# Kernel tuning notes

Hardware: AMD Instinct MI355X
Metric: run time of the kernel (lower is better)

## Reference

```python
import jax, jax.numpy as jnp
import numpy as np

B, T = 4, 2048
IN_H, OUT_H = 4096, 4096   # in_hidden_size = output features, out_hidden_size = input features (torch F.linear quirk)
RANK = 1024


def setup_inputs() -> dict:
    key = jax.random.key(0)
    kx, ku, ks, kv, kb = jax.random.split(key, 5)
    x = jax.random.normal(kx, (B, T, OUT_H), dtype=jnp.float32)
    U = jax.random.normal(ku, (IN_H, RANK), dtype=jnp.float32) * 0.02
    S = jax.random.uniform(ks, (RANK,), dtype=jnp.float32)
    V = jax.random.normal(kv, (OUT_H, RANK), dtype=jnp.float32) * 0.02
    bias = jax.random.normal(kb, (IN_H,), dtype=jnp.float32) * 0.01
    return {"x": x, "U": U, "S": S, "V": V, "bias": bias}


def reference(x, U, S, V, bias):
    # Faithful to torch: M = U @ diag(S) @ V.T  (shape [in_hidden, out_hidden]);
    # F.linear(x, M, bias) = x @ M.T + bias, so x:[...,out_hidden] -> out:[...,in_hidden]
    M = (U * S) @ V.T                     # [IN_H, OUT_H]; (U*S) == U @ diag(S)
    return jnp.einsum('bto,io->bti', x, M) + bias
```

## Files before the change

kernel.cpp:

```cpp
#include <hip/hip_runtime.h>
#include <stdint.h>

typedef __attribute__((ext_vector_type(4))) float  floatx4;
typedef __attribute__((ext_vector_type(8))) short  short8;
typedef __attribute__((ext_vector_type(8))) __bf16 bf16x8;

__device__ __forceinline__ unsigned short f2bf(float f) {
  unsigned int u = __builtin_bit_cast(unsigned int, f);
  u += 0x7fffu + ((u >> 16) & 1u);
  return (unsigned short)(u >> 16);
}

__global__ __launch_bounds__(256) void cast_x_kernel(const float* __restrict__ X,
                                                     unsigned short* __restrict__ Xb) {
  size_t i = ((size_t)blockIdx.x * 256 + threadIdx.x) * 8;
  const floatx4* p = (const floatx4*)(X + i);
  floatx4 a = p[0], b = p[1];
  union { unsigned short us[8]; short8 v; } o;
  o.us[0] = f2bf(a[0]); o.us[1] = f2bf(a[1]); o.us[2] = f2bf(a[2]); o.us[3] = f2bf(a[3]);
  o.us[4] = f2bf(b[0]); o.us[5] = f2bf(b[1]); o.us[6] = f2bf(b[2]); o.us[7] = f2bf(b[3]);
  *(short8*)(Xb + i) = o.v;
}

__global__ __launch_bounds__(256) void transpose_v_kernel(const float* __restrict__ V,
                                                          unsigned short* __restrict__ Vt,
                                                          int rows, int cols) {
  __shared__ float tile[32][33];
  int bx = blockIdx.x * 32;
  int by = blockIdx.y * 32;
  int tx = threadIdx.x & 31;
  int ty = threadIdx.x >> 5;
  for (int i = ty; i < 32; i += 8)
    tile[i][tx] = V[(size_t)(by + i) * cols + bx + tx];
  __syncthreads();
  for (int i = ty; i < 32; i += 8)
    Vt[(size_t)(bx + i) * rows + by + tx] = f2bf(tile[tx][i]);
}

__global__ __launch_bounds__(256) void prep_u_kernel(const float* __restrict__ U,
                                                     const float* __restrict__ S,
                                                     unsigned short* __restrict__ Ub,
                                                     unsigned int rankMask) {
  size_t i = ((size_t)blockIdx.x * 256 + threadIdx.x) * 4;
  floatx4 u = *(const floatx4*)(U + i);
  floatx4 s = *(const floatx4*)(S + (i & (size_t)rankMask));
  union { unsigned short us[4]; unsigned long long v; } o;
  o.us[0] = f2bf(u[0] * s[0]); o.us[1] = f2bf(u[1] * s[1]);
  o.us[2] = f2bf(u[2] * s[2]); o.us[3] = f2bf(u[3] * s[3]);
  *(unsigned long long*)(Ub + i) = o.v;
}

template <bool STORE_BF16>
__global__ __launch_bounds__(256, 2)
void gemm_bt_kernel(const unsigned short* __restrict__ A,
                    const unsigned short* __restrict__ Bt,
                    void* __restrict__ Cv,
                    const float* __restrict__ bias,
                    int M, int N, int K) {
  __shared__ unsigned short sA[128 * 32];
  __shared__ unsigned short sB[128 * 32];

  const int tid  = threadIdx.x;
  const int lane = tid & 63;
  const int wave = tid >> 6;
  const int wm = (wave >> 1) * 64;
  const int wn = (wave & 1) * 64;
  const int row0 = blockIdx.y * 128;
  const int col0 = blockIdx.x * 128;

  floatx4 acc[4][4];
  for (int i = 0; i < 4; ++i)
    for (int j = 0; j < 4; ++j)
      acc[i][j] = (floatx4){0.f, 0.f, 0.f, 0.f};

  const unsigned short* Ablk = A + (size_t)row0 * K;
  const unsigned short* Bblk = Bt + (size_t)col0 * K;

  const int r0 = tid >> 2,         c0 = (tid & 3) * 8;
  const int r1 = (256 + tid) >> 2, c1 = (tid & 3) * 8;
  const int base0 = (wave * 64) * 8;
  const int base1 = (256 + wave * 64) * 8;

  const int mrow = lane & 15;
  const int quad = lane >> 4;

  typedef const __attribute__((address_space(1))) void* gptr_t;
  typedef __attribute__((address_space(3))) void*       lptr_t;

  for (int k0 = 0; k0 < K; k0 += 32) {
    __builtin_amdgcn_global_load_lds((gptr_t)(Ablk + (size_t)r0 * K + k0 + c0),
                                     (lptr_t)(sA + base0), 16, 0, 0);
    __builtin_amdgcn_global_load_lds((gptr_t)(Ablk + (size_t)r1 * K + k0 + c1),
                                     (lptr_t)(sA + base1), 16, 0, 0);
    __builtin_amdgcn_global_load_lds((gptr_t)(Bblk + (size_t)r0 * K + k0 + c0),
                                     (lptr_t)(sB + base0), 16, 0, 0);
    __builtin_amdgcn_global_load_lds((gptr_t)(Bblk + (size_t)r1 * K + k0 + c1),
                                     (lptr_t)(sB + base1), 16, 0, 0);
    __syncthreads();

    bf16x8 af[4], bfr[4];
#pragma unroll
    for (int mi = 0; mi < 4; ++mi)
      af[mi] = __builtin_bit_cast(bf16x8,
                *(const short8*)(sA + (wm + mi * 16 + mrow) * 32 + quad * 8));
#pragma unroll
    for (int ni = 0; ni < 4; ++ni)
      bfr[ni] = __builtin_bit_cast(bf16x8,
                *(const short8*)(sB + (wn + ni * 16 + mrow) * 32 + quad * 8));
#pragma unroll
    for (int mi = 0; mi < 4; ++mi)
#pragma unroll
      for (int ni = 0; ni < 4; ++ni)
        acc[mi][ni] = __builtin_amdgcn_mfma_f32_16x16x32_bf16(af[mi], bfr[ni],
                                                              acc[mi][ni], 0, 0, 0);
    __syncthreads();
  }

  const int orow = row0 + wm + quad * 4;
  const int ocol = col0 + wn + mrow;
  if (STORE_BF16) {
    unsigned short* C = (unsigned short*)Cv;
#pragma unroll
    for (int mi = 0; mi < 4; ++mi)
#pragma unroll
      for (int r = 0; r < 4; ++r) {
        size_t rowoff = (size_t)(orow + mi * 16 + r) * N;
#pragma unroll
        for (int ni = 0; ni < 4; ++ni)
          C[rowoff + ocol + ni * 16] = f2bf(acc[mi][ni][r]);
      }
  } else {
    float* C = (float*)Cv;
    float bv[4];
#pragma unroll
    for (int ni = 0; ni < 4; ++ni) bv[ni] = bias[ocol + ni * 16];
#pragma unroll
    for (int mi = 0; mi < 4; ++mi)
#pragma unroll
      for (int r = 0; r < 4; ++r) {
        size_t rowoff = (size_t)(orow + mi * 16 + r) * N;
#pragma unroll
        for (int ni = 0; ni < 4; ++ni)
          C[rowoff + ocol + ni * 16] = acc[mi][ni][r] + bv[ni];
      }
  }
}

extern "C" void kernel_launch(void* const* d_in, const int* in_sizes, int n_in,
                              void* d_out, int out_size, void* d_ws, size_t ws_size,
                              hipStream_t stream) {
  const float* x    = (const float*)d_in[0];
  const float* U    = (const float*)d_in[1];
  const float* S    = (const float*)d_in[2];
  const float* V    = (const float*)d_in[3];
  const float* bias = (const float*)d_in[4];

  const int RANK = in_sizes[2];
  const int INH  = in_sizes[4];
  const int OUTH = in_sizes[3] / RANK;
  const int M    = in_sizes[0] / OUTH;

  unsigned short* Xb = (unsigned short*)d_ws;
  unsigned short* Vt = Xb + (size_t)M * OUTH;
  unsigned short* Ub = Vt + (size_t)RANK * OUTH;
  unsigned short* Yb = Ub + (size_t)INH * RANK;

  cast_x_kernel<<<(int)(((size_t)M * OUTH) / 2048), 256, 0, stream>>>(x, Xb);
  transpose_v_kernel<<<dim3(RANK / 32, OUTH / 32), 256, 0, stream>>>(V, Vt, OUTH, RANK);
  prep_u_kernel<<<(int)(((size_t)INH * RANK) / 1024), 256, 0, stream>>>(U, S, Ub,
                                                                        (unsigned)(RANK - 1));
  gemm_bt_kernel<true><<<dim3(RANK / 128, M / 128), 256, 0, stream>>>(
      Xb, Vt, (void*)Yb, nullptr, M, RANK, OUTH);
  gemm_bt_kernel<false><<<dim3(INH / 128, M / 128), 256, 0, stream>>>(
      Yb, Ub, d_out, bias, M, INH, RANK);
}
```

Baseline: 430.4 us.

## Fuse prep kernels, swizzle GEMM block order, deepen K step, enlarge GEMM2 tile

Merges the three preprocessing kernels (cast X, transpose V, scale U by S) into one launch that dispatches on block index, cutting launch overhead and tail gaps. Both GEMMs now use a 1D grid with 8-row band swizzling to improve L2 reuse. GEMM1 loads two K-slices per barrier pair, halving sync count. GEMM2 uses 256x128 tiles with 8x4 accumulators per wave for more reuse, at the cost of more registers and fewer blocks.

```diff
diff --git a/kernel.cpp b/kernel.cpp
--- a/kernel.cpp
+++ b/kernel.cpp
@@ -11,96 +11,180 @@
   return (unsigned short)(u >> 16);
 }
 
-__global__ __launch_bounds__(256) void cast_x_kernel(const float* __restrict__ X,
-                                                     unsigned short* __restrict__ Xb) {
-  size_t i = ((size_t)blockIdx.x * 256 + threadIdx.x) * 8;
-  const floatx4* p = (const floatx4*)(X + i);
-  floatx4 a = p[0], b = p[1];
-  union { unsigned short us[8]; short8 v; } o;
-  o.us[0] = f2bf(a[0]); o.us[1] = f2bf(a[1]); o.us[2] = f2bf(a[2]); o.us[3] = f2bf(a[3]);
-  o.us[4] = f2bf(b[0]); o.us[5] = f2bf(b[1]); o.us[6] = f2bf(b[2]); o.us[7] = f2bf(b[3]);
-  *(short8*)(Xb + i) = o.v;
-}
-
-__global__ __launch_bounds__(256) void transpose_v_kernel(const float* __restrict__ V,
-                                                          unsigned short* __restrict__ Vt,
-                                                          int rows, int cols) {
+typedef const __attribute__((address_space(1))) void* gptr_t;
+typedef __attribute__((address_space(3))) void*       lptr_t;
+
+__global__ __launch_bounds__(256) void prep_fused(
+    const float* __restrict__ X, const float* __restrict__ V,
+    const float* __restrict__ U, const float* __restrict__ S,
+    unsigned short* __restrict__ Xb, unsigned short* __restrict__ Vt,
+    unsigned short* __restrict__ Ub,
+    int castBlocks, int transTotal, int transGX, int vrows, int vcols,
+    unsigned int rankMask) {
   __shared__ float tile[32][33];
-  int bx = blockIdx.x * 32;
-  int by = blockIdx.y * 32;
-  int tx = threadIdx.x & 31;
-  int ty = threadIdx.x >> 5;
-  for (int i = ty; i < 32; i += 8)
-    tile[i][tx] = V[(size_t)(by + i) * cols + bx + tx];
-  __syncthreads();
-  for (int i = ty; i < 32; i += 8)
-    Vt[(size_t)(bx + i) * rows + by + tx] = f2bf(tile[tx][i]);
-}
-
-__global__ __launch_bounds__(256) void prep_u_kernel(const float* __restrict__ U,
-                                                     const float* __restrict__ S,
-                                                     unsigned short* __restrict__ Ub,
-                                                     unsigned int rankMask) {
-  size_t i = ((size_t)blockIdx.x * 256 + threadIdx.x) * 4;
-  floatx4 u = *(const floatx4*)(U + i);
-  floatx4 s = *(const floatx4*)(S + (i & (size_t)rankMask));
-  union { unsigned short us[4]; unsigned long long v; } o;
-  o.us[0] = f2bf(u[0] * s[0]); o.us[1] = f2bf(u[1] * s[1]);
-  o.us[2] = f2bf(u[2] * s[2]); o.us[3] = f2bf(u[3] * s[3]);
-  *(unsigned long long*)(Ub + i) = o.v;
-}
-
-template <bool STORE_BF16>
+  int bid = blockIdx.x;
+  int tid = threadIdx.x;
+  if (bid < castBlocks) {
+    size_t i = ((size_t)bid * 256 + tid) * 8;
+    const floatx4* p = (const floatx4*)(X + i);
+    floatx4 a = p[0], b = p[1];
+    union { unsigned short us[8]; short8 v; } o;
+    o.us[0] = f2bf(a[0]); o.us[1] = f2bf(a[1]); o.us[2] = f2bf(a[2]); o.us[3] = f2bf(a[3]);
+    o.us[4] = f2bf(b[0]); o.us[5] = f2bf(b[1]); o.us[6] = f2bf(b[2]); o.us[7] = f2bf(b[3]);
+    *(short8*)(Xb + i) = o.v;
+  } else if (bid < castBlocks + transTotal) {
+    int b  = bid - castBlocks;
+    int bx = (b % transGX) * 32;
+    int by = (b / transGX) * 32;
+    int tx = tid & 31;
+    int ty = tid >> 5;
+    for (int i = ty; i < 32; i += 8)
+      tile[i][tx] = V[(size_t)(by + i) * vcols + bx + tx];
+    __syncthreads();
+    for (int i = ty; i < 32; i += 8)
+      Vt[(size_t)(bx + i) * vrows + by + tx] = f2bf(tile[tx][i]);
+  } else {
+    int b = bid - castBlocks - transTotal;
+    size_t i = ((size_t)b * 256 + tid) * 4;
+    floatx4 u = *(const floatx4*)(U + i);
+    floatx4 s = *(const floatx4*)(S + (i & (size_t)rankMask));
+    union { unsigned short us[4]; unsigned long long v; } o;
+    o.us[0] = f2bf(u[0] * s[0]); o.us[1] = f2bf(u[1] * s[1]);
+    o.us[2] = f2bf(u[2] * s[2]); o.us[3] = f2bf(u[3] * s[3]);
+    *(unsigned long long*)(Ub + i) = o.v;
+  }
+}
+
 __global__ __launch_bounds__(256, 2)
-void gemm_bt_kernel(const unsigned short* __restrict__ A,
-                    const unsigned short* __restrict__ Bt,
-                    void* __restrict__ Cv,
-                    const float* __restrict__ bias,
-                    int M, int N, int K) {
-  __shared__ unsigned short sA[128 * 32];
-  __shared__ unsigned short sB[128 * 32];
+void gemm1_kernel(const unsigned short* __restrict__ A,
+                  const unsigned short* __restrict__ Bt,
+                  unsigned short* __restrict__ C,
+                  int N, int K, int GX) {
+  __shared__ unsigned short sA[2][128 * 32];
+  __shared__ unsigned short sB[2][128 * 32];
 
   const int tid  = threadIdx.x;
   const int lane = tid & 63;
   const int wave = tid >> 6;
   const int wm = (wave >> 1) * 64;
   const int wn = (wave & 1) * 64;
-  const int row0 = blockIdx.y * 128;
-  const int col0 = blockIdx.x * 128;
+
+  unsigned bid  = blockIdx.x;
+  unsigned bw   = 8u * GX;
+  unsigned band = bid / bw, rem = bid % bw;
+  unsigned by   = band * 8 + (rem & 7u);
+  unsigned bx   = rem >> 3;
+  const int row0 = by * 128, col0 = bx * 128;
 
   floatx4 acc[4][4];
+#pragma unroll
   for (int i = 0; i < 4; ++i)
-    for (int j = 0; j < 4; ++j)
-      acc[i][j] = (floatx4){0.f, 0.f, 0.f, 0.f};
+#pragma unroll
+    for (int j = 0; j < 4; ++j) acc[i][j] = (floatx4){0.f, 0.f, 0.f, 0.f};
 
   const unsigned short* Ablk = A + (size_t)row0 * K;
   const unsigned short* Bblk = Bt + (size_t)col0 * K;
 
-  const int r0 = tid >> 2,         c0 = (tid & 3) * 8;
-  const int r1 = (256 + tid) >> 2, c1 = (tid & 3) * 8;
-  const int base0 = (wave * 64) * 8;
-  const int base1 = (256 + wave * 64) * 8;
-
-  const int mrow = lane & 15;
-  const int quad = lane >> 4;
-
-  typedef const __attribute__((address_space(1))) void* gptr_t;
-  typedef __attribute__((address_space(3))) void*       lptr_t;
+  const int r0 = tid >> 2, c0 = (tid & 3) * 8;
+  const int ldso0 = (wave * 64) * 8;
+  const int ldso1 = (256 + wave * 64) * 8;
+  const int mrow = lane & 15, quad = lane >> 4;
+
+  for (int k0 = 0; k0 < K; k0 += 64) {
+#pragma unroll
+    for (int t = 0; t < 2; ++t) {
+      const int kk = k0 + t * 32;
+      __builtin_amdgcn_global_load_lds((gptr_t)(Ablk + (size_t)r0 * K + kk + c0),
+                                       (lptr_t)(sA[t] + ldso0), 16, 0, 0);
+      __builtin_amdgcn_global_load_lds((gptr_t)(Ablk + (size_t)(r0 + 64) * K + kk + c0),
+                                       (lptr_t)(sA[t] + ldso1), 16, 0, 0);
+      __builtin_amdgcn_global_load_lds((gptr_t)(Bblk + (size_t)r0 * K + kk + c0),
+                                       (lptr_t)(sB[t] + ldso0), 16, 0, 0);
+      __builtin_amdgcn_global_load_lds((gptr_t)(Bblk + (size_t)(r0 + 64) * K + kk + c0),
+                                       (lptr_t)(sB[t] + ldso1), 16, 0, 0);
+    }
+    __syncthreads();
+#pragma unroll
+    for (int t = 0; t < 2; ++t) {
+      bf16x8 af[4], bfr[4];
+#pragma unroll
+      for (int mi = 0; mi < 4; ++mi)
+        af[mi] = __builtin_bit_cast(bf16x8,
+                  *(const short8*)(sA[t] + (wm + mi * 16 + mrow) * 32 + quad * 8));
+#pragma unroll
+      for (int ni = 0; ni < 4; ++ni)
+        bfr[ni] = __builtin_bit_cast(bf16x8,
+                  *(const short8*)(sB[t] + (wn + ni * 16 + mrow) * 32 + quad * 8));
+#pragma unroll
+      for (int mi = 0; mi < 4; ++mi)
+#pragma unroll
+        for (int ni = 0; ni < 4; ++ni)
+          acc[mi][ni] = __builtin_amdgcn_mfma_f32_16x16x32_bf16(af[mi], bfr[ni],
+                                                                acc[mi][ni], 0, 0, 0);
+    }
+    __syncthreads();
+  }
+
+  const int orow = row0 + wm + quad * 4;
+  const int ocol = col0 + wn + mrow;
+#pragma unroll
+  for (int mi = 0; mi < 4; ++mi)
+#pragma unroll
+    for (int r = 0; r < 4; ++r) {
+      size_t rowoff = (size_t)(orow + mi * 16 + r) * N;
+#pragma unroll
+      for (int ni = 0; ni < 4; ++ni)
+        C[rowoff + ocol + ni * 16] = f2bf(acc[mi][ni][r]);
+    }
+}
+
+__global__ __launch_bounds__(256, 2)
+void gemm2_kernel(const unsigned short* __restrict__ A,
+                  const unsigned short* __restrict__ Bt,
+                  float* __restrict__ C, const float* __restrict__ bias,
+                  int N, int K, int GX) {
+  __shared__ unsigned short sA[256 * 32];
+  __shared__ unsigned short sB[128 * 32];
+
+  const int tid  = threadIdx.x;
+  const int lane = tid & 63;
+  const int wave = tid >> 6;
+  const int wm = (wave >> 1) * 128;
+  const int wn = (wave & 1) * 64;
+
+  unsigned bid  = blockIdx.x;
+  unsigned bw   = 8u * GX;
+  unsigned band = bid / bw, rem = bid % bw;
+  unsigned by   = band * 8 + (rem & 7u);
+  unsigned bx   = rem >> 3;
+  const int row0 = by * 256, col0 = bx * 128;
+
+  floatx4 acc[8][4];
+#pragma unroll
+  for (int i = 0; i < 8; ++i)
+#pragma unroll
+    for (int j = 0; j < 4; ++j) acc[i][j] = (floatx4){0.f, 0.f, 0.f, 0.f};
+
+  const unsigned short* Ablk = A + (size_t)row0 * K;
+  const unsigned short* Bblk = Bt + (size_t)col0 * K;
+
+  const int r0 = tid >> 2, c0 = (tid & 3) * 8;
+  const int mrow = lane & 15, quad = lane >> 4;
 
   for (int k0 = 0; k0 < K; k0 += 32) {
-    __builtin_amdgcn_global_load_lds((gptr_t)(Ablk + (size_t)r0 * K + k0 + c0),
-                                     (lptr_t)(sA + base0), 16, 0, 0);
-    __builtin_amdgcn_global_load_lds((gptr_t)(Ablk + (size_t)r1 * K + k0 + c1),
-                                     (lptr_t)(sA + base1), 16, 0, 0);
-    __builtin_amdgcn_global_load_lds((gptr_t)(Bblk + (size_t)r0 * K + k0 + c0),
-                                     (lptr_t)(sB + base0), 16, 0, 0);
-    __builtin_amdgcn_global_load_lds((gptr_t)(Bblk + (size_t)r1 * K + k0 + c1),
-                                     (lptr_t)(sB + base1), 16, 0, 0);
-    __syncthreads();
-
-    bf16x8 af[4], bfr[4];
-#pragma unroll
-    for (int mi = 0; mi < 4; ++mi)
+#pragma unroll
+    for (int j = 0; j < 4; ++j)
+      __builtin_amdgcn_global_load_lds((gptr_t)(Ablk + (size_t)(r0 + j * 64) * K + k0 + c0),
+                                       (lptr_t)(sA + (j * 256 + wave * 64) * 8), 16, 0, 0);
+#pragma unroll
+    for (int j = 0; j < 2; ++j)
+      __builtin_amdgcn_global_load_lds((gptr_t)(Bblk + (size_t)(r0 + j * 64) * K + k0 + c0),
+                                       (lptr_t)(sB + (j * 256 + wave * 64) * 8), 16, 0, 0);
+    __syncthreads();
+
+    bf16x8 af[8], bfr[4];
+#pragma unroll
+    for (int mi = 0; mi < 8; ++mi)
       af[mi] = __builtin_bit_cast(bf16x8,
                 *(const short8*)(sA + (wm + mi * 16 + mrow) * 32 + quad * 8));
 #pragma unroll
@@ -108,7 +192,7 @@
       bfr[ni] = __builtin_bit_cast(bf16x8,
                 *(const short8*)(sB + (wn + ni * 16 + mrow) * 32 + quad * 8));
 #pragma unroll
-    for (int mi = 0; mi < 4; ++mi)
+    for (int mi = 0; mi < 8; ++mi)
 #pragma unroll
       for (int ni = 0; ni < 4; ++ni)
         acc[mi][ni] = __builtin_amdgcn_mfma_f32_16x16x32_bf16(af[mi], bfr[ni],
@@ -118,32 +202,18 @@
 
   const int orow = row0 + wm + quad * 4;
   const int ocol = col0 + wn + mrow;
-  if (STORE_BF16) {
-    unsigned short* C = (unsigned short*)Cv;
-#pragma unroll
-    for (int mi = 0; mi < 4; ++mi)
-#pragma unroll
-      for (int r = 0; r < 4; ++r) {
-        size_t rowoff = (size_t)(orow + mi * 16 + r) * N;
-#pragma unroll
-        for (int ni = 0; ni < 4; ++ni)
-          C[rowoff + ocol + ni * 16] = f2bf(acc[mi][ni][r]);
-      }
-  } else {
-    float* C = (float*)Cv;
-    float bv[4];
-#pragma unroll
-    for (int ni = 0; ni < 4; ++ni) bv[ni] = bias[ocol + ni * 16];
-#pragma unroll
-    for (int mi = 0; mi < 4; ++mi)
-#pragma unroll
-      for (int r = 0; r < 4; ++r) {
-        size_t rowoff = (size_t)(orow + mi * 16 + r) * N;
-#pragma unroll
-        for (int ni = 0; ni < 4; ++ni)
-          C[rowoff + ocol + ni * 16] = acc[mi][ni][r] + bv[ni];
-      }
-  }
+  float bv[4];
+#pragma unroll
+  for (int ni = 0; ni < 4; ++ni) bv[ni] = bias[ocol + ni * 16];
+#pragma unroll
+  for (int mi = 0; mi < 8; ++mi)
+#pragma unroll
+    for (int r = 0; r < 4; ++r) {
+      size_t rowoff = (size_t)(orow + mi * 16 + r) * N;
+#pragma unroll
+      for (int ni = 0; ni < 4; ++ni)
+        C[rowoff + ocol + ni * 16] = acc[mi][ni][r] + bv[ni];
+    }
 }
 
 extern "C" void kernel_launch(void* const* d_in, const int* in_sizes, int n_in,
@@ -165,12 +235,17 @@
   unsigned short* Ub = Vt + (size_t)RANK * OUTH;
   unsigned short* Yb = Ub + (size_t)INH * RANK;
 
-  cast_x_kernel<<<(int)(((size_t)M * OUTH) / 2048), 256, 0, stream>>>(x, Xb);
-  transpose_v_kernel<<<dim3(RANK / 32, OUTH / 32), 256, 0, stream>>>(V, Vt, OUTH, RANK);
-  prep_u_kernel<<<(int)(((size_t)INH * RANK) / 1024), 256, 0, stream>>>(U, S, Ub,
-                                                                        (unsigned)(RANK - 1));
-  gemm_bt_kernel<true><<<dim3(RANK / 128, M / 128), 256, 0, stream>>>(
-      Xb, Vt, (void*)Yb, nullptr, M, RANK, OUTH);
-  gemm_bt_kernel<false><<<dim3(INH / 128, M / 128), 256, 0, stream>>>(
-      Yb, Ub, d_out, bias, M, INH, RANK);
-}
+  const int castBlocks = (int)(((size_t)M * OUTH) / 2048);
+  const int transGX    = RANK / 32;
+  const int transTotal = transGX * (OUTH / 32);
+  const int prepUBlk   = (int)(((size_t)INH * RANK) / 1024);
+  prep_fused<<<castBlocks + transTotal + prepUBlk, 256, 0, stream>>>(
+      x, V, U, S, Xb, Vt, Ub, castBlocks, transTotal, transGX, OUTH, RANK,
+      (unsigned)(RANK - 1));
+
+  gemm1_kernel<<<(M / 128) * (RANK / 128), 256, 0, stream>>>(
+      Xb, Vt, Yb, RANK, OUTH, RANK / 128);
+
+  gemm2_kernel<<<(M / 256) * (INH / 128), 256, 0, stream>>>(
+      Yb, Ub, (float*)d_out, bias, INH, RANK, INH / 128);
+}
```

Result: faster. 402.4 us (-6.5%).
